# Performance work log

Measured on AMD Instinct MI355X. Metric: run time of the kernel, lower is better.

## Reference

```python
import jax, jax.numpy as jnp
import numpy as np

N = 30000; F = 16; E = 300000
HD = 256; NH = 8; C = HD // NH; L = 3
S = 256; K = 128
NH_CA = 4; HDC = HD // NH_CA


def _ln(x, g, b):
    mu = jnp.mean(x, -1, keepdims=True)
    v = jnp.mean((x - mu) ** 2, -1, keepdims=True)
    return (x - mu) / jnp.sqrt(v + 1e-5) * g + b


def setup_inputs() -> dict:
    ks = iter(jax.random.split(jax.random.key(0), 64))
    def nrm(sh, s=0.05):
        return jax.random.normal(next(ks), sh, jnp.float32) * s
    def zeros(sh):
        return jnp.zeros(sh, jnp.float32)
    def ones(sh):
        return jnp.ones(sh, jnp.float32)
    inp = {}
    inp['x'] = jax.random.normal(next(ks), (N, F), jnp.float32)
    inp['edge_index'] = jax.random.randint(next(ks), (2, E), 0, N, jnp.int32)
    inp['batch'] = jnp.zeros((N,), jnp.int32)
    inp['sheet_node_idx'] = jax.random.randint(next(ks), (S, K), 0, N, jnp.int32)
    inp['sheet_features'] = jax.random.normal(next(ks), (S, F), jnp.float32)
    # pre_transform
    inp['pre_W'] = nrm((F, HD)); inp['pre_b'] = zeros((HD,))
    # stacked GATv2 layers (lin_l, lin_r, att, bias)
    inp['gat_Wl'] = nrm((L, HD, HD)); inp['gat_Wr'] = nrm((L, HD, HD))
    inp['gat_att'] = nrm((L, NH, C)); inp['gat_b'] = zeros((L, HD))
    # geometry encoder
    inp['geo_W1'] = nrm((F, HD)); inp['geo_b1'] = zeros((HD,))
    inp['geo_g1'] = ones((HD,)); inp['geo_be1'] = zeros((HD,))
    inp['geo_W2'] = nrm((HD, HD)); inp['geo_b2'] = zeros((HD,))
    inp['geo_g2'] = ones((HD,)); inp['geo_be2'] = zeros((HD,))
    # cross attention (4 heads)
    inp['ca_Wq'] = nrm((HD, HD)); inp['ca_bq'] = zeros((HD,))
    inp['ca_Wk'] = nrm((HD, HD)); inp['ca_bk'] = zeros((HD,))
    inp['ca_Wv'] = nrm((HD, HD)); inp['ca_bv'] = zeros((HD,))
    inp['ca_Wo'] = nrm((HD, HD)); inp['ca_bo'] = zeros((HD,))
    # q_mlp
    inp['q_W1'] = nrm((2 * HD, HD)); inp['q_b1'] = zeros((HD,))
    inp['q_g1'] = ones((HD,)); inp['q_be1'] = zeros((HD,))
    inp['q_W2'] = nrm((HD, HD // 2)); inp['q_b2'] = zeros((HD // 2,))
    inp['q_g2'] = ones((HD // 2,)); inp['q_be2'] = zeros((HD // 2,))
    inp['q_W3'] = nrm((HD // 2, 1)); inp['q_b3'] = zeros((1,))
    # state_done_predictor
    inp['d_W1'] = nrm((HD, HD // 2)); inp['d_b1'] = zeros((HD // 2,))
    inp['d_g1'] = ones((HD // 2,)); inp['d_be1'] = zeros((HD // 2,))
    inp['d_W2'] = nrm((HD // 2, 1)); inp['d_b2'] = zeros((1,))
    return inp


def _fwd(x, sheet_features, pre_W, pre_b, gat_Wl, gat_Wr, gat_att, gat_b,
         geo_W1, geo_b1, geo_g1, geo_be1, geo_W2, geo_b2, geo_g2, geo_be2,
         ca_Wq, ca_bq, ca_Wk, ca_bk, ca_Wv, ca_bv, ca_Wo, ca_bo,
         q_W1, q_b1, q_g1, q_be1, q_W2, q_b2, q_g2, q_be2, q_W3, q_b3,
         d_W1, d_b1, d_g1, d_be1, d_W2, d_b2,
         edge_index, batch, sheet_node_idx):
    loops = jnp.arange(N, dtype=edge_index.dtype)  # PyG GATv2Conv add_self_loops=True
    src = jnp.concatenate([edge_index[0], loops])
    dst = jnp.concatenate([edge_index[1], loops])
    h = x @ pre_W + pre_b  # [N, HD]
    for l in range(L):
        xl = (h @ gat_Wl[l]).reshape(N, NH, C)  # source messages
        xr = (h @ gat_Wr[l]).reshape(N, NH, C)  # target
        m = jax.nn.leaky_relu(xl[src] + xr[dst], 0.2)  # [E+N, NH, C]
        e = jnp.einsum('ehc,hc->eh', m, gat_att[l])
        emax = jax.ops.segment_max(e, dst, num_segments=N)
        a = jnp.exp(e - emax[dst])
        denom = jax.ops.segment_sum(a, dst, num_segments=N)
        alpha = a / (denom[dst] + 1e-16)  # scatter softmax over incoming edges
        h = jax.ops.segment_sum(alpha[:, :, None] * xl[src], dst, num_segments=N)
        h = jax.nn.elu(h.reshape(N, HD) + gat_b[l])
    cnt = jax.ops.segment_sum(jnp.ones((N,), h.dtype), batch, num_segments=1)
    g = jax.ops.segment_sum(h, batch, num_segments=1) / cnt[:, None]  # [1, HD]
    sheet = h[sheet_node_idx].mean(axis=1)  # [S, HD] per-sheet gather+mean
    geo = jax.nn.relu(_ln(sheet_features @ geo_W1 + geo_b1, geo_g1, geo_be1))
    geo = jax.nn.relu(_ln(geo @ geo_W2 + geo_b2, geo_g2, geo_be2))
    qh = (sheet @ ca_Wq + ca_bq).reshape(S, NH_CA, HDC)
    kh = (geo @ ca_Wk + ca_bk).reshape(S, NH_CA, HDC)
    vh = (geo @ ca_Wv + ca_bv).reshape(S, NH_CA, HDC)
    att = jax.nn.softmax(jnp.einsum('qhd,khd->hqk', qh, kh) / jnp.sqrt(jnp.float32(HDC)), axis=-1)
    fused = jnp.einsum('hqk,khd->qhd', att, vh).reshape(S, HD) @ ca_Wo + ca_bo
    hq = jnp.concatenate([fused, jnp.broadcast_to(g, (S, HD))], axis=1)  # [S, 2*HD]
    hq = jax.nn.relu(_ln(hq @ q_W1 + q_b1, q_g1, q_be1))
    hq = jax.nn.relu(_ln(hq @ q_W2 + q_b2, q_g2, q_be2))
    q_values = (hq @ q_W3 + q_b3)[:, 0]  # [S]
    hd = jax.nn.relu(_ln(g @ d_W1 + d_b1, d_g1, d_be1))
    done_logit = (hd @ d_W2 + d_b2)[:, 0]  # [1]
    return q_values, done_logit


def reference(x, edge_index, batch, sheet_node_idx, sheet_features, pre_W, pre_b,
              gat_Wl, gat_Wr, gat_att, gat_b,
              geo_W1, geo_b1, geo_g1, geo_be1, geo_W2, geo_b2, geo_g2, geo_be2,
              ca_Wq, ca_bq, ca_Wk, ca_bk, ca_Wv, ca_bv, ca_Wo, ca_bo,
              q_W1, q_b1, q_g1, q_be1, q_W2, q_b2, q_g2, q_be2, q_W3, q_b3,
              d_W1, d_b1, d_g1, d_be1, d_W2, d_b2):
    return _fwd(x, sheet_features, pre_W, pre_b, gat_Wl, gat_Wr, gat_att, gat_b,
                geo_W1, geo_b1, geo_g1, geo_be1, geo_W2, geo_b2, geo_g2, geo_be2,
                ca_Wq, ca_bq, ca_Wk, ca_bk, ca_Wv, ca_bv, ca_Wo, ca_bo,
                q_W1, q_b1, q_g1, q_be1, q_W2, q_b2, q_g2, q_be2, q_W3, q_b3,
                d_W1, d_b1, d_g1, d_be1, d_W2, d_b2,
                edge_index, batch, sheet_node_idx)
```

## Files before the change

### kernel.cpp

```cpp
#include <hip/hip_runtime.h>
#include <hip/hip_bf16.h>
#include <stdint.h>

#define NN 30000
#define MPAD 30080
#define FI 16
#define EE 300000
#define ETOT (EE + NN)
#define HD 256
#define NH 8
#define CH 32
#define NL 3
#define SS 256
#define KS 128
#define NHC 4
#define HC 64
#define GSB 256
#define RPB 118
#define SCB 118

typedef _Float16 half8 __attribute__((ext_vector_type(8)));
typedef _Float16 half4v __attribute__((ext_vector_type(4)));
typedef _Float16 half2v __attribute__((ext_vector_type(2)));
typedef float f32x4 __attribute__((ext_vector_type(4)));

__device__ __forceinline__ float wsum(float v) {
#pragma unroll
  for (int d = 1; d < 64; d <<= 1) v += __shfl_xor(v, d);
  return v;
}

__device__ __forceinline__ half2v mk2(_Float16 a, _Float16 b) {
  half2v r; r[0] = a; r[1] = b; return r;
}

__device__ __forceinline__ half2v h2max(half2v a, half2v b) {
#if __has_builtin(__builtin_elementwise_max)
  return __builtin_elementwise_max(a, b);
#else
  half2v r; r[0] = a[0] > b[0] ? a[0] : b[0]; r[1] = a[1] > b[1] ? a[1] : b[1];
  return r;
#endif
}

__device__ __forceinline__ float h2dot(half2v a, half2v b, float c) {
#if __has_builtin(__builtin_amdgcn_fdot2)
  return __builtin_amdgcn_fdot2(a, b, c, false);
#else
  return c + (float)a[0] * (float)b[0] + (float)a[1] * (float)b[1];
#endif
}

__device__ __forceinline__ float ln_fast(float a, int t, int n, float* red16,
    const float* __restrict__ G, const float* __restrict__ Be, bool relu)
{
  float av = (t < n) ? a : 0.f;
  float s = wsum(av), s2 = wsum(av * av);
  if ((t & 63) == 0) { red16[t >> 6] = s; red16[8 + (t >> 6)] = s2; }
  __syncthreads();
  float sum = red16[0] + red16[1] + red16[2] + red16[3];
  float sq  = red16[8] + red16[9] + red16[10] + red16[11];
  float mu = sum / n;
  float var = sq / n - mu * mu;
  float o = 0.f;
  if (t < n) {
    o = (a - mu) * rsqrtf(var + 1e-5f) * G[t] + Be[t];
    if (relu) o = fmaxf(o, 0.f);
  }
  __syncthreads();
  return o;
}

__global__ __launch_bounds__(256) void k_init(int* __restrict__ cnt,
    int* __restrict__ gcnt, _Float16* __restrict__ h16pad, int* __restrict__ csr_pad)
{
  int i = blockIdx.x * 256 + threadIdx.x;
  if (i < NN) cnt[i] = 0;
  if (i == 0) gcnt[0] = 0;
  if (i < 8) csr_pad[i] = 0;
  if (i < (MPAD - NN) * HD) h16pad[i] = (_Float16)0.f;
}

__global__ __launch_bounds__(256) void k_wconvAll(
    const float* __restrict__ Wl, const float* __restrict__ Wr,
    const float* __restrict__ geo_W2, const float* __restrict__ ca_Wq,
    const float* __restrict__ ca_Wk, const float* __restrict__ ca_Wv,
    const float* __restrict__ ca_Wo, const float* __restrict__ q_W1,
    const float* __restrict__ q_W2,
    _Float16* __restrict__ WT,
    _Float16* __restrict__ Tgeo2, _Float16* __restrict__ Tq,
    _Float16* __restrict__ Tk, _Float16* __restrict__ Tv,
    _Float16* __restrict__ To, _Float16* __restrict__ Tq1,
    _Float16* __restrict__ Tq2)
{
  int b = blockIdx.x, t = threadIdx.x;
  if (b < 1536) {
    int m = b >> 8;
    int n = b & 255;
    int l = m >> 1;
    const float* W = (m & 1) ? (Wr + (size_t)l * HD * HD) : (Wl + (size_t)l * HD * HD);
    WT[((size_t)m * HD + n) * HD + t] = (_Float16)W[t * HD + n];
    return;
  }
  b -= 1536;
  if (b < 1280) {
    int seg = b >> 8;
    int n = b & 255;
    const float* src = (seg == 0) ? geo_W2 : (seg == 1) ? ca_Wq : (seg == 2) ? ca_Wk
                     : (seg == 3) ? ca_Wv : ca_Wo;
    _Float16* dst = (seg == 0) ? Tgeo2 : (seg == 1) ? Tq : (seg == 2) ? Tk
                  : (seg == 3) ? Tv : To;
    dst[(size_t)n * 256 + t] = (_Float16)src[(size_t)t * 256 + n];
  } else if (b < 1536) {
    int n = b - 1280;
    Tq1[(size_t)n * 512 + t]       = (_Float16)q_W1[(size_t)t * 256 + n];
    Tq1[(size_t)n * 512 + 256 + t] = (_Float16)q_W1[(size_t)(256 + t) * 256 + n];
  } else {
    int n = b - 1536;
    Tq2[(size_t)n * 256 + t] = (_Float16)q_W2[(size_t)t * 128 + n];
  }
}

__global__ __launch_bounds__(256) void k_pre(const float* __restrict__ x,
    const float* __restrict__ W, const float* __restrict__ b,
    _Float16* __restrict__ H16)
{
  __shared__ float Ws[FI][HD];
  __shared__ float xs[8][FI];
  int r0 = blockIdx.x * 8;
  int t = threadIdx.x;
  for (int i = t; i < FI * HD; i += 256) Ws[i >> 8][i & 255] = W[i];
  if (t < 8 * FI) xs[t >> 4][t & 15] = x[(size_t)(r0 + (t >> 4)) * FI + (t & 15)];
  __syncthreads();
  float bj = b[t];
  for (int r = 0; r < 8; ++r) {
    float acc = bj;
#pragma unroll
    for (int k = 0; k < FI; ++k) acc += xs[r][k] * Ws[k][t];
    H16[(size_t)(r0 + r) * HD + t] = (_Float16)acc;
  }
}

__global__ __launch_bounds__(256) void k_count(const int* __restrict__ ei, int* __restrict__ cnt)
{
  int i = blockIdx.x * 256 + threadIdx.x;
  if (i >= ETOT) return;
  int dst = (i < EE) ? ei[EE + i] : (i - EE);
  atomicAdd(&cnt[dst], 1);
}

__global__ __launch_bounds__(256) void k_scanA(const int* __restrict__ cnt,
    int* __restrict__ rowptr, int* __restrict__ btot)
{
  __shared__ int wt[4];
  int b = blockIdx.x, t = threadIdx.x;
  int i = b * 256 + t;
  int v = (i < NN) ? cnt[i] : 0;
  int lane = t & 63, w = t >> 6;
  int s = v;
#pragma unroll
  for (int d = 1; d < 64; d <<= 1) {
    int u = __shfl_up(s, d);
    if (lane >= d) s += u;
  }
  if (lane == 63) wt[w] = s;
  __syncthreads();
  int off = 0;
  for (int k = 0; k < w; ++k) off += wt[k];
  if (i < NN) rowptr[i] = off + s - v;
  if (t == 255) btot[b] = off + s;
}

__global__ __launch_bounds__(128) void k_scanB(const int* __restrict__ btot,
    int* __restrict__ boff, int* __restrict__ rowptr)
{
  __shared__ int wt[2];
  int t = threadIdx.x;
  int v = (t < SCB) ? btot[t] : 0;
  int lane = t & 63, w = t >> 6;
  int s = v;
#pragma unroll
  for (int d = 1; d < 64; d <<= 1) {
    int u = __shfl_up(s, d);
    if (lane >= d) s += u;
  }
  if (lane == 63) wt[w] = s;
  __syncthreads();
  int off = (w == 1) ? wt[0] : 0;
  if (t < SCB) boff[t] = off + s - v;
  if (t == 127) rowptr[NN] = wt[0] + wt[1];
}

__global__ __launch_bounds__(256) void k_scanC(int* __restrict__ rowptr,
    const int* __restrict__ boff, int* __restrict__ wptr)
{
  int b = blockIdx.x, t = threadIdx.x;
  int i = b * 256 + t;
  if (i < NN) {
    int r = rowptr[i] + boff[b];
    rowptr[i] = r;
    wptr[i] = r;
  }
}

__global__ __launch_bounds__(256) void k_scatter(const int* __restrict__ ei,
    int* __restrict__ wptr, int* __restrict__ csr_src)
{
  int i = blockIdx.x * 256 + threadIdx.x;
  if (i >= ETOT) return;
  int src = (i < EE) ? ei[i] : (i - EE);
  int dst = (i < EE) ? ei[EE + i] : (i - EE);
  int pos = atomicAdd(&wptr[dst], 1);
  csr_src[pos] = src;
}

#define BK 64
__global__ __launch_bounds__(256) void k_gemm16(const _Float16* __restrict__ A,
    const _Float16* __restrict__ WT,
    _Float16* __restrict__ Xl, _Float16* __restrict__ Xr)
{
  __shared__ __align__(16) _Float16 As[128 * BK];
  __shared__ __align__(16) _Float16 Bs[128 * BK];
  int t = threadIdx.x;
  int w = t >> 6, lane = t & 63;
  int row0 = blockIdx.x * 128;
  int ct = blockIdx.y;
  const _Float16* Bmat = WT + (size_t)(ct >> 1) * HD * HD + (size_t)(ct & 1) * 128 * HD;
  _Float16* Out = (ct >> 1) ? Xr : Xl;
  int j0 = (ct & 1) * 128;

  f32x4 acc[4][4] = {};
  int wr = w >> 1, wc = w & 1;

  for (int k0 = 0; k0 < HD; k0 += BK) {
#pragma unroll
    for (int i = 0; i < 4; ++i) {
      int p = (i * 4 + w) * 64 + lane;
      int row = p >> 3, s = p & 7;
      int g = s ^ (row & 7);
      const _Float16* srcA = A + (size_t)(row0 + row) * HD + k0 + g * 8;
      __builtin_amdgcn_global_load_lds(
        (const __attribute__((address_space(1))) void*)srcA,
        (__attribute__((address_space(3))) void*)((char*)As + (i * 4 + w) * 1024),
        16, 0, 0);
      const _Float16* srcB = Bmat + (size_t)row * HD + k0 + g * 8;
      __builtin_amdgcn_global_load_lds(
        (const __attribute__((address_space(1))) void*)srcB,
        (__attribute__((address_space(3))) void*)((char*)Bs + (i * 4 + w) * 1024),
        16, 0, 0);
    }
    __syncthreads();
#pragma unroll
    for (int ks = 0; ks < 2; ++ks) {
      half8 af[4], bfr[4];
      int kslot = ks * 4 + (lane >> 4);
#pragma unroll
      for (int mi = 0; mi < 4; ++mi) {
        int rl = wr * 64 + mi * 16 + (lane & 15);
        int ps = kslot ^ (rl & 7);
        af[mi] = *(const half8*)((const char*)As + rl * 128 + ps * 16);
      }
#pragma unroll
      for (int ni = 0; ni < 4; ++ni) {
        int nl = wc * 64 + ni * 16 + (lane & 15);
        int ps = kslot ^ (nl & 7);
        bfr[ni] = *(const half8*)((const char*)Bs + nl * 128 + ps * 16);
      }
#pragma unroll
      for (int mi = 0; mi < 4; ++mi)
#pragma unroll
        for (int ni = 0; ni < 4; ++ni)
          acc[mi][ni] = __builtin_amdgcn_mfma_f32_16x16x32_f16(af[mi], bfr[ni], acc[mi][ni], 0, 0, 0);
    }
    __syncthreads();
  }
  int crow = (lane >> 4) * 4;
  int ccol = lane & 15;
#pragma unroll
  for (int mi = 0; mi < 4; ++mi)
#pragma unroll
    for (int ni = 0; ni < 4; ++ni) {
      size_t base_r = row0 + wr * 64 + mi * 16 + crow;
      int c = j0 + wc * 64 + ni * 16 + ccol;
#pragma unroll
      for (int r = 0; r < 4; ++r)
        Out[(base_r + r) * HD + c] = (_Float16)acc[mi][ni][r];
    }
}

__global__ __launch_bounds__(256) void k_edgeagg(const _Float16* __restrict__ Xl,
    const _Float16* __restrict__ Xr, const float* __restrict__ attw,
    const float* __restrict__ bias, const int* __restrict__ rowptr,
    const int* __restrict__ csr_src, _Float16* __restrict__ H16)
{
  int node = blockIdx.x * 4 + (threadIdx.x >> 6);
  int lane = threadIdx.x & 63;
  if (node >= NN) return;
  int st = rowptr[node], en = rowptr[node + 1];
  int n = en - st;
  int hf = lane >> 5, sl = lane & 31;
  int c = sl * 8;
  half8 xrv = *(const half8*)(Xr + (size_t)node * HD + c);
  float4 wa = *(const float4*)(attw + c);
  float4 wb = *(const float4*)(attw + c + 4);
  half2v w0 = mk2((_Float16)wa.x, (_Float16)wa.y);
  half2v w1 = mk2((_Float16)wa.z, (_Float16)wa.w);
  half2v w2 = mk2((_Float16)wb.x, (_Float16)wb.y);
  half2v w3 = mk2((_Float16)wb.z, (_Float16)wb.w);
  half2v r0 = mk2(xrv[0], xrv[1]), r1 = mk2(xrv[2], xrv[3]);
  half2v r2 = mk2(xrv[4], xrv[5]), r3 = mk2(xrv[6], xrv[7]);
  half2v c02 = mk2((_Float16)0.2f, (_Float16)0.2f);

  float mh = -1e30f, dsum = 0.f;
  float a[8] = {};
  int trips = (n + 1) >> 1;

  int idx0 = csr_src[st + hf];
  half8 xv = *(const half8*)(Xl + (size_t)idx0 * HD + c);

  for (int it = 0; it < trips; ++it) {
    bool valid = (2 * it + hf) < n;
    half8 xc = xv;
    if (it + 1 < trips) {
      int nidx = csr_src[st + 2 * (it + 1) + hf];
      xv = *(const half8*)(Xl + (size_t)nidx * HD + c);
    }
    half2v x0 = mk2(xc[0], xc[1]), x1 = mk2(xc[2], xc[3]);
    half2v x2 = mk2(xc[4], xc[5]), x3 = mk2(xc[6], xc[7]);
    half2v s0 = x0 + r0, s1 = x1 + r1, s2 = x2 + r2, s3 = x3 + r3;
    half2v m0 = h2max(s0, s0 * c02);
    half2v m1 = h2max(s1, s1 * c02);
    half2v m2 = h2max(s2, s2 * c02);
    half2v m3 = h2max(s3, s3 * c02);
    float e = h2dot(m3, w3, h2dot(m2, w2, h2dot(m1, w1, h2dot(m0, w0, 0.f))));
    e += __shfl_xor(e, 1);
    e += __shfl_xor(e, 2);
    e = valid ? e : -1e30f;
    if (__any(e > mh + 8.f)) {
      float nm = fmaxf(mh, e);
      float sc = __expf(mh - nm);
      dsum *= sc;
#pragma unroll
      for (int j = 0; j < 8; ++j) a[j] *= sc;
      mh = nm;
    }
    float pw = valid ? __expf(e - mh) : 0.f;
#pragma unroll
    for (int j = 0; j < 8; ++j) a[j] += pw * (float)xc[j];
    dsum += pw;
  }
  float om = __shfl_xor(mh, 32);
  float od = __shfl_xor(dsum, 32);
  float nm = fmaxf(mh, om);
  float scs = __expf(mh - nm);
  float sco = __expf(om - nm);
  float d = dsum * scs + od * sco;
#pragma unroll
  for (int j = 0; j < 8; ++j) {
    float oa = __shfl_xor(a[j], 32);
    a[j] = a[j] * scs + oa * sco;
  }
  if (hf == 0) {
    float inv = 1.f / (d + 1e-16f);
    float4 ba = *(const float4*)(bias + c);
    float4 bb = *(const float4*)(bias + c + 4);
    float ob[8] = {ba.x, ba.y, ba.z, ba.w, bb.x, bb.y, bb.z, bb.w};
    half8 h8;
#pragma unroll
    for (int j = 0; j < 8; ++j) {
      float o = a[j] * inv + ob[j];
      o = (o > 0.f) ? o : expm1f(o);
      h8[j] = (_Float16)o;
    }
    *(half8*)(H16 + (size_t)node * HD + c) = h8;
  }
}

__global__ __launch_bounds__(256) void k_gsum(const _Float16* __restrict__ H,
    const int* __restrict__ batch, float* __restrict__ gpart, int* __restrict__ gcnt)
{
  __shared__ float flagf[RPB];
  __shared__ int scount;
  int b = blockIdx.x, t = threadIdx.x;
  int r0 = b * RPB;
  int nr = NN - r0; if (nr > RPB) nr = RPB; if (nr < 0) nr = 0;
  if (t == 0) scount = 0;
  __syncthreads();
  if (t < nr) {
    int ok = (batch[r0 + t] == 0) ? 1 : 0;
    flagf[t] = (float)ok;
    if (ok) atomicAdd(&scount, 1);
  }
  __syncthreads();
  float a0 = 0.f, a1 = 0.f, a2 = 0.f, a3 = 0.f;
  const _Float16* Hp = H + (size_t)r0 * HD + t;
  int r = 0;
  for (; r + 4 <= nr; r += 4) {
    float v0 = (float)Hp[(size_t)(r + 0) * HD];
    float v1 = (float)Hp[(size_t)(r + 1) * HD];
    float v2 = (float)Hp[(size_t)(r + 2) * HD];
    float v3 = (float)Hp[(size_t)(r + 3) * HD];
    a0 += v0 * flagf[r + 0]; a1 += v1 * flagf[r + 1];
    a2 += v2 * flagf[r + 2]; a3 += v3 * flagf[r + 3];
  }
  for (; r < nr; ++r) a0 += (float)Hp[(size_t)r * HD] * flagf[r];
  gpart[(size_t)b * HD + t] = (a0 + a1) + (a2 + a3);
  if (t == 0 && scount) atomicAdd(gcnt, scount);
}

__global__ __launch_bounds__(256) void k_tail1(const _Float16* __restrict__ h16,
    const int* __restrict__ sheet_idx, const float* __restrict__ sheet_feat,
    const float* __restrict__ geo_W1, const float* __restrict__ geo_b1,
    const float* __restrict__ geo_g1, const float* __restrict__ geo_be1,
    const float* __restrict__ gpart, const int* __restrict__ gcnt,
    float* __restrict__ gvec,
    _Float16* __restrict__ sh16, _Float16* __restrict__ g116)
{
  __shared__ float xf[FI];
  __shared__ int sidx[KS];
  __shared__ float red16[16];
  int s = blockIdx.x, t = threadIdx.x;

  if (s == SS) {
    float a0 = 0.f, a1 = 0.f, a2 = 0.f, a3 = 0.f;
    for (int b = 0; b < GSB; b += 4) {
      a0 += gpart[(size_t)b * HD + t];
      a1 += gpart[(size_t)(b + 1) * HD + t];
      a2 += gpart[(size_t)(b + 2) * HD + t];
      a3 += gpart[(size_t)(b + 3) * HD + t];
    }
    gvec[t] = ((a0 + a1) + (a2 + a3)) / (float)(*gcnt);
    return;
  }

  if (t < KS) sidx[t] = sheet_idx[s * KS + t];
  if (t >= 240) xf[t - 240] = sheet_feat[s * FI + (t - 240)];
  __syncthreads();

  float pa[8] = {};
#pragma unroll 2
  for (int r = 0; r < KS; r += 8) {
#pragma unroll
    for (int u = 0; u < 8; ++u)
      pa[u] += (float)h16[(size_t)sidx[r + u] * HD + t];
  }
  float shv = ((pa[0] + pa[1]) + (pa[2] + pa[3]) + (pa[4] + pa[5]) + (pa[6] + pa[7])) * (1.f / KS);
  sh16[(size_t)s * HD + t] = (_Float16)shv;

  float a = geo_b1[t];
#pragma unroll
  for (int k = 0; k < FI; ++k) a += xf[k] * geo_W1[k * HD + t];
  float g1 = ln_fast(a, t, 256, red16, geo_g1, geo_be1, true);
  g116[(size_t)s * HD + t] = (_Float16)g1;
}

template <int KD, int NW>
__global__ __launch_bounds__(NW * 64) void k_stageLN(
    const _Float16* __restrict__ X, const _Float16* __restrict__ WT,
    const float* __restrict__ b, const float* __restrict__ G,
    const float* __restrict__ Be, _Float16* __restrict__ Y,
    const float* __restrict__ W3, const float* __restrict__ b3,
    float* __restrict__ outq,
    const float* __restrict__ gvec,
    const float* __restrict__ dW1, const float* __restrict__ db1,
    const float* __restrict__ dg1, const float* __restrict__ dbe1,
    const float* __restrict__ dW2, const float* __restrict__ db2,
    float* __restrict__ outd)
{
  __shared__ float ps[NW * 16], ps2[NW * 16], pq[NW * 16];
  const int NCOL = NW * 64;
  int t = threadIdx.x;

  if (outd != nullptr && blockIdx.x == 16) {
    int w2 = t >> 6;
    float acc2 = db1[t];
    for (int k = 0; k < 256; ++k) acc2 += gvec[k] * dW1[(size_t)k * 128 + t];
    float s = wsum(acc2), s2v = wsum(acc2 * acc2);
    if ((t & 63) == 0) { ps[w2] = s; ps2[w2] = s2v; }
    __syncthreads();
    float S = ps[0] + ps[1], S2 = ps2[0] + ps2[1];
    float mu = S * (1.f / 128.f), var = S2 * (1.f / 128.f) - mu * mu;
    float hdv = fmaxf((acc2 - mu) * rsqrtf(var + 1e-5f) * dg1[t] + dbe1[t], 0.f);
    float o = wsum(hdv * dW2[t]);
    if ((t & 63) == 0) pq[w2] = o;
    __syncthreads();
    if (t == 0) outd[0] = pq[0] + pq[1] + db2[0];
    return;
  }

  int w = t >> 6, lane = t & 63;
  int arow = lane & 15, kg = lane >> 4;
  int m0 = blockIdx.x * 16;
  int col0 = w * 64;

  f32x4 acc[4] = {};
#pragma unroll
  for (int ks = 0; ks < KD / 32; ++ks) {
    half8 af = *(const half8*)(X + (size_t)(m0 + arow) * KD + ks * 32 + kg * 8);
#pragma unroll
    for (int n = 0; n < 4; ++n) {
      half8 bf = *(const half8*)(WT + (size_t)(col0 + n * 16 + arow) * KD + ks * 32 + kg * 8);
      acc[n] = __builtin_amdgcn_mfma_f32_16x16x32_f16(af, bf, acc[n], 0, 0, 0);
    }
  }
#pragma unroll
  for (int n = 0; n < 4; ++n) {
    float bv = b[col0 + n * 16 + arow];
#pragma unroll
    for (int r = 0; r < 4; ++r) acc[n][r] += bv;
  }
  float s[4] = {}, s2[4] = {};
#pragma unroll
  for (int n = 0; n < 4; ++n)
#pragma unroll
    for (int r = 0; r < 4; ++r) { float v = acc[n][r]; s[r] += v; s2[r] += v * v; }
#pragma unroll
  for (int d = 1; d < 16; d <<= 1)
#pragma unroll
    for (int r = 0; r < 4; ++r) { s[r] += __shfl_xor(s[r], d); s2[r] += __shfl_xor(s2[r], d); }
  if (arow == 0) {
#pragma unroll
    for (int r = 0; r < 4; ++r) {
      ps[w * 16 + kg * 4 + r] = s[r];
      ps2[w * 16 + kg * 4 + r] = s2[r];
    }
  }
  __syncthreads();
  float mu[4], rs[4];
#pragma unroll
  for (int r = 0; r < 4; ++r) {
    float S = 0.f, S2 = 0.f;
#pragma unroll
    for (int w2 = 0; w2 < NW; ++w2) { S += ps[w2 * 16 + kg * 4 + r]; S2 += ps2[w2 * 16 + kg * 4 + r]; }
    float m = S / NCOL;
    float var = S2 / NCOL - m * m;
    mu[r] = m; rs[r] = rsqrtf(var + 1e-5f);
  }
#pragma unroll
  for (int n = 0; n < 4; ++n) {
    int col = col0 + n * 16 + arow;
    float gv = G[col], bev = Be[col];
#pragma unroll
    for (int r = 0; r < 4; ++r)
      acc[n][r] = fmaxf((acc[n][r] - mu[r]) * rs[r] * gv + bev, 0.f);
  }
  if (Y) {
#pragma unroll
    for (int n = 0; n < 4; ++n) {
      int col = col0 + n * 16 + arow;
#pragma unroll
      for (int r = 0; r < 4; ++r)
        Y[(size_t)(m0 + kg * 4 + r) * NCOL + col] = (_Float16)acc[n][r];
    }
  }
  if (outq) {
    float p[4] = {};
#pragma unroll
    for (int n = 0; n < 4; ++n) {
      float w3 = W3[col0 + n * 16 + arow];
#pragma unroll
      for (int r = 0; r < 4; ++r) p[r] += acc[n][r] * w3;
    }
#pragma unroll
    for (int d = 1; d < 16; d <<= 1)
#pragma unroll
      for (int r = 0; r < 4; ++r) p[r] += __shfl_xor(p[r], d);
    if (arow == 0)
#pragma unroll
      for (int r = 0; r < 4; ++r) pq[w * 16 + kg * 4 + r] = p[r];
    __syncthreads();
    if (w == 0 && arow == 0) {
#pragma unroll
      for (int r = 0; r < 4; ++r) {
        float o = b3[0];
#pragma unroll
        for (int w2 = 0; w2 < NW; ++w2) o += pq[w2 * 16 + kg * 4 + r];
        outq[m0 + kg * 4 + r] = o;
      }
    }
  }
}

__global__ __launch_bounds__(64) void k_qkv(
    const _Float16* __restrict__ sh16, const _Float16* __restrict__ g216,
    const _Float16* __restrict__ Tq, const _Float16* __restrict__ Tk,
    const _Float16* __restrict__ Tv,
    const float* __restrict__ bq, const float* __restrict__ bk,
    const float* __restrict__ bv,
    _Float16* __restrict__ qb, _Float16* __restrict__ kb, _Float16* __restrict__ vb)
{
  int lane = threadIdx.x;
  int arow = lane & 15, kg = lane >> 4;
  int m0 = blockIdx.x * 16;
  int col0 = blockIdx.y * 64;
  int mat = blockIdx.z;
  const _Float16* X = (mat == 0) ? sh16 : g216;
  const _Float16* WT = (mat == 0) ? Tq : (mat == 1) ? Tk : Tv;
  const float* b = (mat == 0) ? bq : (mat == 1) ? bk : bv;
  _Float16* Y = (mat == 0) ? qb : (mat == 1) ? kb : vb;

  f32x4 acc[4] = {};
#pragma unroll
  for (int ks = 0; ks < 8; ++ks) {
    half8 af = *(const half8*)(X + (size_t)(m0 + arow) * 256 + ks * 32 + kg * 8);
#pragma unroll
    for (int n = 0; n < 4; ++n) {
      half8 bf = *(const half8*)(WT + (size_t)(col0 + n * 16 + arow) * 256 + ks * 32 + kg * 8);
      acc[n] = __builtin_amdgcn_mfma_f32_16x16x32_f16(af, bf, acc[n], 0, 0, 0);
    }
  }
#pragma unroll
  for (int n = 0; n < 4; ++n) {
    int col = col0 + n * 16 + arow;
    float bv2 = b[col];
#pragma unroll
    for (int r = 0; r < 4; ++r)
      Y[(size_t)(m0 + kg * 4 + r) * 256 + col] = (_Float16)(acc[n][r] + bv2);
  }
}

__global__ __launch_bounds__(64) void k_wo(
    const _Float16* __restrict__ pv16, const _Float16* __restrict__ To,
    const float* __restrict__ bo, const float* __restrict__ gvec,
    _Float16* __restrict__ hqin)
{
  int lane = threadIdx.x;
  int arow = lane & 15, kg = lane >> 4;
  int m0 = blockIdx.x * 16;
  int col0 = blockIdx.y * 64;

  f32x4 acc[4] = {};
#pragma unroll
  for (int ks = 0; ks < 8; ++ks) {
    half8 af = *(const half8*)(pv16 + (size_t)(m0 + arow) * 256 + ks * 32 + kg * 8);
#pragma unroll
    for (int n = 0; n < 4; ++n) {
      half8 bf = *(const half8*)(To + (size_t)(col0 + n * 16 + arow) * 256 + ks * 32 + kg * 8);
      acc[n] = __builtin_amdgcn_mfma_f32_16x16x32_f16(af, bf, acc[n], 0, 0, 0);
    }
  }
#pragma unroll
  for (int n = 0; n < 4; ++n) {
    int col = col0 + n * 16 + arow;
    float bv = bo[col];
    _Float16 gg = (_Float16)gvec[col];
#pragma unroll
    for (int r = 0; r < 4; ++r) {
      hqin[(size_t)(m0 + kg * 4 + r) * 512 + col] = (_Float16)(acc[n][r] + bv);
      hqin[(size_t)(m0 + kg * 4 + r) * 512 + 256 + col] = gg;
    }
  }
}

__global__ __launch_bounds__(1024) void k_attn(const _Float16* __restrict__ qb,
    const _Float16* __restrict__ kb, const _Float16* __restrict__ vb,
    _Float16* __restrict__ pv16)
{
  __shared__ float qv[HD];
  __shared__ float att[1024];
  __shared__ float red4[1024];
  __shared__ float redm[16];
  __shared__ float reds[16];
  int row = blockIdx.x, t = threadIdx.x;
  int w = t >> 6;

  if (t < 256) qv[t] = (float)qb[(size_t)row * HD + t];
  __syncthreads();

  int h = t >> 8, key = t & 255;
  float e = 0.f;
  {
    const half8* kr = (const half8*)(kb + (size_t)key * HD + h * HC);
    const float* qh = qv + h * HC;
#pragma unroll
    for (int d = 0; d < 8; ++d) {
      half8 kk = kr[d];
#pragma unroll
      for (int u = 0; u < 8; ++u) e += qh[d * 8 + u] * (float)kk[u];
    }
    e *= 0.125f;
  }
  float wm = e;
#pragma unroll
  for (int d = 1; d < 64; d <<= 1) wm = fmaxf(wm, __shfl_xor(wm, d));
  if ((t & 63) == 0) redm[w] = wm;
  __syncthreads();
  float mx = fmaxf(fmaxf(redm[4 * h], redm[4 * h + 1]), fmaxf(redm[4 * h + 2], redm[4 * h + 3]));
  float pw = __expf(e - mx);
  float ws = wsum(pw);
  if ((t & 63) == 0) reds[w] = ws;
  att[t] = pw;
  __syncthreads();

  int kq = t >> 8, j = t & 255;
  int hj = j >> 6;
  float p = 0.f;
  const float* arow = att + hj * 256 + kq * 64;
  const _Float16* vcol = vb + (size_t)(kq * 64) * HD + j;
  for (int k = 0; k < 64; ++k)
    p += arow[k] * (float)vcol[(size_t)k * HD];
  red4[t] = p;
  __syncthreads();
  if (t < 256) {
    int hh = t >> 6;
    float dsum = reds[4 * hh] + reds[4 * hh + 1] + reds[4 * hh + 2] + reds[4 * hh + 3];
    float pv = (red4[t] + red4[256 + t] + red4[512 + t] + red4[768 + t]) / dsum;
    pv16[(size_t)row * HD + t] = (_Float16)pv;
  }
}

extern "C" void kernel_launch(void* const* d_in, const int* in_sizes, int n_in,
                              void* d_out, int out_size, void* d_ws, size_t ws_size,
                              hipStream_t stream) {
  const float* x      = (const float*)d_in[0];
  const int*   ei     = (const int*)d_in[1];
  const int*   batch  = (const int*)d_in[2];
  const int*   sheet_idx = (const int*)d_in[3];
  const float* sheet_feat = (const float*)d_in[4];
  const float* pre_W  = (const float*)d_in[5];
  const float* pre_b  = (const float*)d_in[6];
  const float* gat_Wl = (const float*)d_in[7];
  const float* gat_Wr = (const float*)d_in[8];
  const float* gat_att = (const float*)d_in[9];
  const float* gat_b  = (const float*)d_in[10];
  const float* geo_W1 = (const float*)d_in[11];
  const float* geo_b1 = (const float*)d_in[12];
  const float* geo_g1 = (const float*)d_in[13];
  const float* geo_be1 = (const float*)d_in[14];
  const float* geo_W2 = (const float*)d_in[15];
  const float* geo_b2 = (const float*)d_in[16];
  const float* geo_g2 = (const float*)d_in[17];
  const float* geo_be2 = (const float*)d_in[18];
  const float* ca_Wq = (const float*)d_in[19];
  const float* ca_bq = (const float*)d_in[20];
  const float* ca_Wk = (const float*)d_in[21];
  const float* ca_bk = (const float*)d_in[22];
  const float* ca_Wv = (const float*)d_in[23];
  const float* ca_bv = (const float*)d_in[24];
  const float* ca_Wo = (const float*)d_in[25];
  const float* ca_bo = (const float*)d_in[26];
  const float* q_W1 = (const float*)d_in[27];
  const float* q_b1 = (const float*)d_in[28];
  const float* q_g1 = (const float*)d_in[29];
  const float* q_be1 = (const float*)d_in[30];
  const float* q_W2 = (const float*)d_in[31];
  const float* q_b2 = (const float*)d_in[32];
  const float* q_g2 = (const float*)d_in[33];
  const float* q_be2 = (const float*)d_in[34];
  const float* q_W3 = (const float*)d_in[35];
  const float* q_b3 = (const float*)d_in[36];
  const float* d_W1 = (const float*)d_in[37];
  const float* d_b1 = (const float*)d_in[38];
  const float* d_g1 = (const float*)d_in[39];
  const float* d_be1 = (const float*)d_in[40];
  const float* d_W2 = (const float*)d_in[41];
  const float* d_b2 = (const float*)d_in[42];

  char* wsb = (char*)d_ws;
  auto alloc = [&](size_t bytes) { char* p = wsb; wsb += (bytes + 255) & ~(size_t)255; return p; };

  _Float16* h16  = (_Float16*)alloc((size_t)MPAD * HD * 2);
  _Float16* Xl16 = (_Float16*)alloc((size_t)MPAD * HD * 2);
  _Float16* Xr16 = (_Float16*)alloc((size_t)MPAD * HD * 2);
  _Float16* WT   = (_Float16*)alloc((size_t)6 * HD * HD * 2);
  _Float16* Tgeo2 = (_Float16*)alloc((size_t)HD * HD * 2);
  _Float16* Tq   = (_Float16*)alloc((size_t)HD * HD * 2);
  _Float16* Tk   = (_Float16*)alloc((size_t)HD * HD * 2);
  _Float16* Tv   = (_Float16*)alloc((size_t)HD * HD * 2);
  _Float16* To   = (_Float16*)alloc((size_t)HD * HD * 2);
  _Float16* Tq1  = (_Float16*)alloc((size_t)HD * 512 * 2);
  _Float16* Tq2  = (_Float16*)alloc((size_t)128 * HD * 2);
  _Float16* sh16 = (_Float16*)alloc((size_t)SS * HD * 2);
  _Float16* g116 = (_Float16*)alloc((size_t)SS * HD * 2);
  _Float16* g216 = (_Float16*)alloc((size_t)SS * HD * 2);
  _Float16* qb16 = (_Float16*)alloc((size_t)SS * HD * 2);
  _Float16* kb16 = (_Float16*)alloc((size_t)SS * HD * 2);
  _Float16* vb16 = (_Float16*)alloc((size_t)SS * HD * 2);
  _Float16* pv16 = (_Float16*)alloc((size_t)SS * HD * 2);
  _Float16* hqin16 = (_Float16*)alloc((size_t)SS * 512 * 2);
  _Float16* hq116 = (_Float16*)alloc((size_t)SS * HD * 2);
  float* gpart   = (float*)alloc((size_t)GSB * HD * 4);
  float* gvec    = (float*)alloc(256 * 4);
  int* cnt       = (int*)alloc((size_t)NN * 4);
  int* rowptr    = (int*)alloc((size_t)(NN + 1) * 4);
  int* wptr      = (int*)alloc((size_t)NN * 4);
  int* csr_src   = (int*)alloc((size_t)(ETOT + 8) * 4);
  int* btot      = (int*)alloc((size_t)SCB * 4);
  int* boff      = (int*)alloc((size_t)SCB * 4);
  int* gcnt      = (int*)alloc(4);

  float* out_q = (float*)d_out;
  float* out_d = out_q + SS;

  k_init<<<118, 256, 0, stream>>>(cnt, gcnt, h16 + (size_t)NN * HD, csr_src + ETOT);

  k_count<<<(ETOT + 255) / 256, 256, 0, stream>>>(ei, cnt);
  k_scanA<<<SCB, 256, 0, stream>>>(cnt, rowptr, btot);
  k_scanB<<<1, 128, 0, stream>>>(btot, boff, rowptr);
  k_scanC<<<SCB, 256, 0, stream>>>(rowptr, boff, wptr);
  k_scatter<<<(ETOT + 255) / 256, 256, 0, stream>>>(ei, wptr, csr_src);

  k_wconvAll<<<3200, 256, 0, stream>>>(gat_Wl, gat_Wr, geo_W2, ca_Wq, ca_Wk, ca_Wv,
                                       ca_Wo, q_W1, q_W2,
                                       WT, Tgeo2, Tq, Tk, Tv, To, Tq1, Tq2);
  k_pre<<<NN / 8, 256, 0, stream>>>(x, pre_W, pre_b, h16);

  dim3 ggrid(MPAD / 128, 4);
  for (int l = 0; l < NL; ++l) {
    k_gemm16<<<ggrid, 256, 0, stream>>>(h16, WT + (size_t)l * 2 * HD * HD, Xl16, Xr16);
    k_edgeagg<<<(NN + 3) / 4, 256, 0, stream>>>(Xl16, Xr16, gat_att + l * NH * CH,
                                                gat_b + l * HD, rowptr, csr_src, h16);
  }

  k_gsum<<<GSB, 256, 0, stream>>>(h16, batch, gpart, gcnt);

  k_tail1<<<SS + 1, 256, 0, stream>>>(h16, sheet_idx, sheet_feat,
      geo_W1, geo_b1, geo_g1, geo_be1, gpart, gcnt, gvec, sh16, g116);
  k_stageLN<256, 4><<<16, 256, 0, stream>>>(g116, Tgeo2, geo_b2, geo_g2, geo_be2,
      g216, nullptr, nullptr, nullptr,
      nullptr, nullptr, nullptr, nullptr, nullptr, nullptr, nullptr, nullptr);
  dim3 qkvg(16, 4, 3);
  k_qkv<<<qkvg, 64, 0, stream>>>(sh16, g216, Tq, Tk, Tv, ca_bq, ca_bk, ca_bv,
                                 qb16, kb16, vb16);
  k_attn<<<SS, 1024, 0, stream>>>(qb16, kb16, vb16, pv16);
  dim3 wog(16, 4);
  k_wo<<<wog, 64, 0, stream>>>(pv16, To, ca_bo, gvec, hqin16);
  k_stageLN<512, 4><<<16, 256, 0, stream>>>(hqin16, Tq1, q_b1, q_g1, q_be1,
      hq116, nullptr, nullptr, nullptr,
      nullptr, nullptr, nullptr, nullptr, nullptr, nullptr, nullptr, nullptr);
  k_stageLN<256, 2><<<17, 128, 0, stream>>>(hq116, Tq2, q_b2, q_g2, q_be2,
      nullptr, q_W3, q_b3, out_q,
      gvec, d_W1, d_b1, d_g1, d_be1, d_W2, d_b2, out_d);
}
```

Baseline: 309.4 us.

## Widen GATv2 GEMM tile to full width and deepen edge gather prefetch

The layer GEMM now uses 512-thread blocks that each compute a 128x256 output tile, covering the full output width. Each A tile is loaded once instead of twice, and the grid in y shrinks from 4 to 2. The edge aggregation kernel keeps three neighbour feature rows in flight instead of one, to hide gather latency, and splits the attention dot product into two independent chains. The prefetch condition is always true, so each node reads a few csr_src entries past its own range, and past the array end for the last nodes. That relies on padding after csr_src, and the larger GEMM blocks raise LDS and register use per block.

```diff
diff --git a/kernel.cpp b/kernel.cpp
--- a/kernel.cpp
+++ b/kernel.cpp
@@ -214,39 +214,42 @@
   csr_src[pos] = src;
 }
 
-#define BK 64
-__global__ __launch_bounds__(256) void k_gemm16(const _Float16* __restrict__ A,
+#define BKG 64
+__global__ __launch_bounds__(512) void k_gemm16(const _Float16* __restrict__ A,
     const _Float16* __restrict__ WT,
     _Float16* __restrict__ Xl, _Float16* __restrict__ Xr)
 {
-  __shared__ __align__(16) _Float16 As[128 * BK];
-  __shared__ __align__(16) _Float16 Bs[128 * BK];
+  __shared__ __align__(16) _Float16 As[128 * BKG];
+  __shared__ __align__(16) _Float16 Bs[256 * BKG];
   int t = threadIdx.x;
   int w = t >> 6, lane = t & 63;
   int row0 = blockIdx.x * 128;
   int ct = blockIdx.y;
-  const _Float16* Bmat = WT + (size_t)(ct >> 1) * HD * HD + (size_t)(ct & 1) * 128 * HD;
-  _Float16* Out = (ct >> 1) ? Xr : Xl;
-  int j0 = (ct & 1) * 128;
+  const _Float16* Bmat = WT + (size_t)ct * HD * HD;
+  _Float16* Out = ct ? Xr : Xl;
 
   f32x4 acc[4][4] = {};
-  int wr = w >> 1, wc = w & 1;
-
-  for (int k0 = 0; k0 < HD; k0 += BK) {
-#pragma unroll
-    for (int i = 0; i < 4; ++i) {
-      int p = (i * 4 + w) * 64 + lane;
+  int wr = w >> 2, wc = w & 3;
+
+  for (int k0 = 0; k0 < HD; k0 += BKG) {
+#pragma unroll
+    for (int i = 0; i < 2; ++i) {
+      int p = i * 512 + t;
       int row = p >> 3, s = p & 7;
       int g = s ^ (row & 7);
-      const _Float16* srcA = A + (size_t)(row0 + row) * HD + k0 + g * 8;
       __builtin_amdgcn_global_load_lds(
-        (const __attribute__((address_space(1))) void*)srcA,
-        (__attribute__((address_space(3))) void*)((char*)As + (i * 4 + w) * 1024),
+        (const __attribute__((address_space(1))) void*)(A + (size_t)(row0 + row) * HD + k0 + g * 8),
+        (__attribute__((address_space(3))) void*)((char*)As + (i * 8 + w) * 1024),
         16, 0, 0);
-      const _Float16* srcB = Bmat + (size_t)row * HD + k0 + g * 8;
+    }
+#pragma unroll
+    for (int i = 0; i < 4; ++i) {
+      int p = i * 512 + t;
+      int row = p >> 3, s = p & 7;
+      int g = s ^ (row & 7);
       __builtin_amdgcn_global_load_lds(
-        (const __attribute__((address_space(1))) void*)srcB,
-        (__attribute__((address_space(3))) void*)((char*)Bs + (i * 4 + w) * 1024),
+        (const __attribute__((address_space(1))) void*)(Bmat + (size_t)row * HD + k0 + g * 8),
+        (__attribute__((address_space(3))) void*)((char*)Bs + (i * 8 + w) * 1024),
         16, 0, 0);
     }
     __syncthreads();
@@ -281,7 +284,7 @@
 #pragma unroll
     for (int ni = 0; ni < 4; ++ni) {
       size_t base_r = row0 + wr * 64 + mi * 16 + crow;
-      int c = j0 + wc * 64 + ni * 16 + ccol;
+      int c = wc * 64 + ni * 16 + ccol;
 #pragma unroll
       for (int r = 0; r < 4; ++r)
         Out[(base_r + r) * HD + c] = (_Float16)acc[mi][ni][r];
@@ -314,16 +317,19 @@
   float mh = -1e30f, dsum = 0.f;
   float a[8] = {};
   int trips = (n + 1) >> 1;
-
-  int idx0 = csr_src[st + hf];
-  half8 xv = *(const half8*)(Xl + (size_t)idx0 * HD + c);
+  int base = st + hf;
+
+  half8 b0 = *(const half8*)(Xl + (size_t)csr_src[base] * HD + c);
+  half8 b1 = *(const half8*)(Xl + (size_t)csr_src[base + 2] * HD + c);
+  half8 b2 = *(const half8*)(Xl + (size_t)csr_src[base + 4] * HD + c);
 
   for (int it = 0; it < trips; ++it) {
     bool valid = (2 * it + hf) < n;
-    half8 xc = xv;
-    if (it + 1 < trips) {
-      int nidx = csr_src[st + 2 * (it + 1) + hf];
-      xv = *(const half8*)(Xl + (size_t)nidx * HD + c);
+    half8 xc = b0;
+    b0 = b1; b1 = b2;
+    if (it + 3 < trips + 3) {
+      int nidx = csr_src[base + 2 * (it + 3)];
+      b2 = *(const half8*)(Xl + (size_t)nidx * HD + c);
     }
     half2v x0 = mk2(xc[0], xc[1]), x1 = mk2(xc[2], xc[3]);
     half2v x2 = mk2(xc[4], xc[5]), x3 = mk2(xc[6], xc[7]);
@@ -332,7 +338,9 @@
     half2v m1 = h2max(s1, s1 * c02);
     half2v m2 = h2max(s2, s2 * c02);
     half2v m3 = h2max(s3, s3 * c02);
-    float e = h2dot(m3, w3, h2dot(m2, w2, h2dot(m1, w1, h2dot(m0, w0, 0.f))));
+    float eA = h2dot(m1, w1, h2dot(m0, w0, 0.f));
+    float eB = h2dot(m3, w3, h2dot(m2, w2, 0.f));
+    float e = eA + eB;
     e += __shfl_xor(e, 1);
     e += __shfl_xor(e, 2);
     e = valid ? e : -1e30f;
@@ -805,9 +813,9 @@
                                        WT, Tgeo2, Tq, Tk, Tv, To, Tq1, Tq2);
   k_pre<<<NN / 8, 256, 0, stream>>>(x, pre_W, pre_b, h16);
 
-  dim3 ggrid(MPAD / 128, 4);
+  dim3 ggrid(MPAD / 128, 2);
   for (int l = 0; l < NL; ++l) {
-    k_gemm16<<<ggrid, 256, 0, stream>>>(h16, WT + (size_t)l * 2 * HD * HD, Xl16, Xr16);
+    k_gemm16<<<ggrid, 512, 0, stream>>>(h16, WT + (size_t)l * 2 * HD * HD, Xl16, Xr16);
     k_edgeagg<<<(NN + 3) / 4, 256, 0, stream>>>(Xl16, Xr16, gat_att + l * NH * CH,
                                                 gat_b + l * HD, rowptr, csr_src, h16);
   }
```

Result: no change. 305.6 us (-1.2%).
